# Kernel optimization log

Hardware: AMD Instinct MI355X
Metric: run time of the kernel (lower is better)

## Reference

```python
import jax, jax.numpy as jnp
import numpy as np

# dims
B, L, D = 2, 2048, 768
K, KQ, M = 12, 6, 4          # heads, query heads, thetas
H = D // K                    # 64 head dim (expand_factor=1)
NREP = K // KQ                # 2
MEM = K * H                   # 768
FLAT = K * H * M              # 3072
EXP = H * 3                   # 192 (out_expand_factor=3)
DSW = EXP * 2                 # 384 swiglu per head
LAT = D // 4                  # 192
CK = 4                        # conv kernel size
TH_MIN, TH_MAX = 1e-3, 3.0


def setup_inputs() -> dict:
    key = jax.random.key(0)
    ks = jax.random.split(key, 10)
    rn = lambda k, sh, s=0.02: jax.random.normal(k, sh, jnp.float32) * s
    # faithful parameter inits from the flax module
    grid_m = np.geomspace(TH_MIN, TH_MAX, M)
    theta_d_raw = jnp.asarray(
        np.log(np.exp(np.tile(grid_m.reshape(1, 1, 1, 1, M), (1, 1, K, H, 1))) - 1.0 + 1e-4),
        jnp.float32)
    decay_slopes = jnp.asarray(np.log(np.exp(np.geomspace(1e-3, 0.1, K)) - 1.0), jnp.float32)
    return {
        "x": jax.random.normal(ks[0], (B, L, D), jnp.float32),
        "W_mem": rn(ks[1], (D, MEM + K)),
        "conv_k": rn(ks[2], (CK, 1, MEM + K), 0.2),
        "W_q": rn(ks[3], (D, KQ * H * M * 2)),
        "theta_d_raw": theta_d_raw,
        "decay_slopes": decay_slopes,
        "score_scale": jnp.ones((K,), jnp.float32),
        "tanh_scale": jnp.ones((K,), jnp.float32),
        "W_re": rn(ks[4], (K, H, DSW), 0.05),
        "W_im": rn(ks[5], (K, H, DSW), 0.05),
        "norm_scale": jnp.ones((1, 1, K, H), jnp.float32),
        "gate_W": jnp.zeros((D, K), jnp.float32),
        "gate_b": jnp.full((K,), -3.0, jnp.float32),
        "skip_down_W": rn(ks[6], (D, LAT)),
        "skip_up_W": rn(ks[7], (LAT, K * DSW)),
        "highway_scale": jnp.ones((1, 1, K, 1), jnp.float32),
        "out_W": rn(ks[8], (K * EXP, D)),
    }


def reference(x, W_mem, conv_k, W_q, theta_d_raw, decay_slopes, score_scale, tanh_scale,
              W_re, W_im, norm_scale, gate_W, gate_b, skip_down_W, skip_up_W,
              highway_scale, out_W):
    b, l, _ = x.shape
    # memory stream: dense proj + depthwise causal conv
    z = x @ W_mem                                                     # (b,l,MEM+K)
    z = jax.lax.conv_general_dilated(z, conv_k, (1,), [(CK - 1, 0)],
                                     dimension_numbers=('NWC', 'WIO', 'NWC'),
                                     feature_group_count=MEM + K)
    k_val = z[..., :MEM].reshape(b, l, K, H)
    s_raw = z[..., MEM:].reshape(b, l, K, 1)
    q = (x @ W_q).reshape(b, l, KQ, H, M, 2)
    q_re, q_im = q[..., 0], q[..., 1]
    # multi-frequency theta grid + trapezoid quadrature weights
    theta_d = jax.nn.softplus(theta_d_raw) + 1e-4
    ta = jnp.cumsum(theta_d, axis=-1)
    total = ta[..., -1:]
    rng = TH_MAX - TH_MIN
    theta = TH_MIN + ta / total * rng                                 # (1,1,K,H,M)
    dth = (ta[..., 1:] - ta[..., :-1]) * (rng / total)
    w_int = jnp.concatenate([dth[..., :1] * 0.5,
                             0.5 * (dth[..., :-1] + dth[..., 1:]),
                             dth[..., -1:] * 0.5], axis=-1)           # (1,1,K,H,M)
    # ALiBi-like decay anchored at sequence end (all decay heads)
    pos = jnp.arange(l, dtype=jnp.float32)
    slopes = jax.nn.softplus(decay_slopes).reshape(1, 1, K, 1)
    dist = jnp.maximum(jnp.float32(l - 1) - pos, 0.0)
    log_tw = -slopes * dist[None, :, None, None]                      # (1,l,K,1)
    log_p = jnp.clip(score_scale[None, None, :, None] * s_raw, -20.0, 20.0)
    p_w = jnp.exp(log_p + log_tw)                                     # (b,l,K,1)
    # complex rotation of keys by per-head/per-freq phase
    kvw = k_val[..., None] * p_w[..., None]                           # (b,l,K,H,1)
    phi = jnp.tanh(tanh_scale.reshape(1, 1, K, 1, 1) * k_val[..., None]) * theta  # (b,l,K,H,M)
    re_k = kvw * jnp.cos(phi)
    im_k = kvw * jnp.sin(phi)
    # fused prefix-sum over time of (denominator, Re, Im)
    merged = jnp.concatenate([p_w[..., 0],
                              re_k.reshape(b, l, FLAT),
                              im_k.reshape(b, l, FLAT)], axis=-1)
    cs = jnp.cumsum(merged, axis=1)
    den, num_re, num_im = cs[..., :K], cs[..., K:K + FLAT], cs[..., K + FLAT:]
    inv_den = 1.0 / jnp.maximum(den[..., None], 1e-4)                 # (b,l,K,1)
    s_re = (num_re.reshape(b, l, K, H, M) * inv_den[..., None]).reshape(b, l, KQ, NREP, H, M)
    s_im = (num_im.reshape(b, l, K, H, M) * inv_den[..., None]).reshape(b, l, KQ, NREP, H, M)
    w_g = w_int.reshape(1, 1, KQ, NREP, H, M)
    qr, qi = q_re[:, :, :, None], q_im[:, :, :, None]                 # GQA broadcast over n_rep
    out_re = jnp.sum((s_re * qr + s_im * qi) * w_g, axis=-1).reshape(b, l, K, H)
    out_im = jnp.sum((s_im * qr - s_re * qi) * w_g, axis=-1).reshape(b, l, K, H)
    # gated spectral output + low-rank highway skip, swiglu, out proj
    gate = jax.nn.sigmoid(x @ gate_W + gate_b)[..., None]             # (b,l,K,1)
    y_re = jnp.einsum('blkh,khn->blkn', out_re * norm_scale, W_re)
    y_im = jnp.einsum('blkh,khn->blkn', out_im * norm_scale, W_im)
    y_spec = (y_re + y_im) * gate                                     # (b,l,K,DSW)
    y_dir = ((x @ skip_down_W) @ skip_up_W).reshape(b, l, K, DSW)
    yv_s, yg_s = jnp.split(y_spec, 2, axis=-1)
    yv_d, yg_d = jnp.split(y_dir, 2, axis=-1)
    y_val = yv_s + yv_d * highway_scale
    y_gate = yg_s + yg_d * highway_scale
    y = (y_val * jax.nn.silu(y_gate)).reshape(b, l, K * EXP)
    return y @ out_W
```

## Files before the change

kernel.cpp:

```cpp
#include <hip/hip_runtime.h>
#include <math.h>

#define B_    2
#define L_    2048
#define D_    768
#define K_    12
#define KQ_   6
#define M_    4
#define H_    64
#define ZC_   780
#define NTOK_ 4096
#define NC_   64
#define LC_   32
#define QST_  3072
#define XPN_  4096
#define ZOFF_ 3276

typedef __attribute__((ext_vector_type(8))) _Float16 half8;
typedef __attribute__((ext_vector_type(4))) float f32x4;

__device__ __forceinline__ float softplus_f(float x) {
  return (x > 20.f) ? x : log1pf(expf(x));
}

__device__ __forceinline__ float fast_tanh(float x) {
  float xx = fminf(fmaxf(x, -10.f), 10.f);
  float e = __expf(2.f * xx);
  return (e - 1.f) / (e + 1.f);
}

__device__ __forceinline__ void async16(const _Float16* g, _Float16* l) {
  __builtin_amdgcn_global_load_lds(
      (const __attribute__((address_space(1))) unsigned int*)g,
      (__attribute__((address_space(3))) unsigned int*)l, 16, 0, 0);
}

__device__ __forceinline__ int permcol(int n) {
  int isg = (n >= 192) ? 1 : 0;
  int j = n - 192 * isg;
  return (j >> 4) * 32 + (isg << 4) + (j & 15);
}

#define FENCE() asm volatile("" ::: "memory")

__device__ __forceinline__ void cvt_t_body(float (*tile)[33], int bx, int by, int kz,
                                           const float* src, long sKs, int srs,
                                           _Float16* dh, long dKs, int dst, int doff,
                                           int R, int Nact, int Nst, bool perm, float scale) {
  const float* s = src + (size_t)kz * sKs;
  _Float16* dhh = dh + (size_t)kz * dKs;
  const int kb = bx * 32;
  const int nb = by * 32;
  const int tx = threadIdx.x & 31, ty = threadIdx.x >> 5;
  for (int i = ty; i < 32; i += 8) {
    int kk = kb + i, n = nb + tx;
    tile[i][tx] = (kk < R && n < Nact) ? s[(size_t)kk * srs + n] : 0.f;
  }
  __syncthreads();
  for (int i = ty; i < 32; i += 8) {
    int n = nb + i, kk = kb + tx;
    if (kk < R && n < Nst) {
      float v = tile[tx][i] * scale;
      int dn = perm ? permcol(n) : n;
      dhh[(size_t)dn * dst + doff + kk] = (_Float16)v;
    }
  }
}

__global__ __launch_bounds__(256)
void prep_kernel(const float* __restrict__ x,
                 const float* __restrict__ W_mem, const float* __restrict__ W_q,
                 const float* __restrict__ skip_down_W, const float* __restrict__ out_W,
                 const float* __restrict__ W_re, const float* __restrict__ W_im,
                 const float* __restrict__ skip_up_W, const float* __restrict__ hs,
                 const float* __restrict__ gate_W,
                 const float* __restrict__ theta_d_raw, const float* __restrict__ decay,
                 _Float16* __restrict__ x_h,
                 _Float16* __restrict__ xpb_h, _Float16* __restrict__ outw_h,
                 _Float16* __restrict__ bsp_h,
                 float* __restrict__ theta_tab, float* __restrict__ w_tab,
                 float* __restrict__ slopes_sp) {
  __shared__ float tile[32][33];
  int b = blockIdx.x;
  if (b < 3) {
    int idx = b * 256 + threadIdx.x;
    if (idx < K_) slopes_sp[idx] = softplus_f(decay[idx]);
    if (idx >= K_ * H_) return;
    float td[M_], ta[M_];
#pragma unroll
    for (int m = 0; m < M_; ++m) td[m] = softplus_f(theta_d_raw[idx * M_ + m]) + 1e-4f;
    ta[0] = td[0];
#pragma unroll
    for (int m = 1; m < M_; ++m) ta[m] = ta[m - 1] + td[m];
    float total = ta[M_ - 1];
    float rs = 2.999f / total;
#pragma unroll
    for (int m = 0; m < M_; ++m) theta_tab[idx * M_ + m] = 0.001f + ta[m] * rs;
    float d0 = (ta[1] - ta[0]) * rs;
    float d1 = (ta[2] - ta[1]) * rs;
    float d2 = (ta[3] - ta[2]) * rs;
    w_tab[idx * M_ + 0] = 0.5f * d0;
    w_tab[idx * M_ + 1] = 0.5f * (d0 + d1);
    w_tab[idx * M_ + 2] = 0.5f * (d1 + d2);
    w_tab[idx * M_ + 3] = 0.5f * d2;
    return;
  }
  b -= 3;
  if (b < 6360) {
    if (b < 672) {
      cvt_t_body(tile, b % 24, b / 24, 0, W_mem, 0, ZC_, xpb_h + (size_t)ZOFF_ * 768,
                 0, 768, 0, 768, ZC_, ZC_, false, 1.f);
      return;
    }
    b -= 672;
    if (b < 2304) {
      cvt_t_body(tile, b % 24, b / 24, 0, W_q, 0, 3072, xpb_h, 0, 768, 0, 768,
                 3072, 3072, false, 1.f);
      return;
    }
    b -= 2304;
    if (b < 192) {
      cvt_t_body(tile, b % 24, b / 24, 0, skip_down_W, 0, 192, xpb_h + (size_t)3072 * 768,
                 0, 768, 0, 768, 192, 192, false, 1.f);
      return;
    }
    b -= 192;
    if (b < 1728) {
      cvt_t_body(tile, b % 72, b / 72, 0, out_W, 0, 768, outw_h, 0, 2304, 0, 2304,
                 768, 768, false, 1.f);
      return;
    }
    b -= 1728;
    if (b < 288) {
      cvt_t_body(tile, b % 2, (b / 2) % 12, b / 24, W_re, 64L * 384, 384, bsp_h,
                 384L * 320, 320, 0, 64, 384, 384, true, 1.f);
      return;
    }
    b -= 288;
    if (b < 288) {
      cvt_t_body(tile, b % 2, (b / 2) % 12, b / 24, W_im, 64L * 384, 384, bsp_h,
                 384L * 320, 320, 64, 64, 384, 384, true, 1.f);
      return;
    }
    b -= 288;
    if (b < 864) {
      int kz = b / 72;
      cvt_t_body(tile, b % 6, (b / 6) % 12, kz, skip_up_W, 384, 4608, bsp_h,
                 384L * 320, 320, 128, 192, 384, 384, true, hs[kz]);
      return;
    }
    b -= 864;
    cvt_t_body(tile, b, 0, 0, gate_W, 0, K_, xpb_h + (size_t)3264 * 768,
               0, 768, 0, 768, K_, K_, false, 1.f);
    return;
  }
  b -= 6360;
  size_t i = (size_t)b * 256 + threadIdx.x;
  if (i < (size_t)NTOK_ * D_) {
    x_h[i] = (_Float16)x[i];
  }
}

__global__ __launch_bounds__(512, 2)
void xproj256_kernel(const _Float16* __restrict__ Ah, const _Float16* __restrict__ Bh,
                     float* __restrict__ C, _Float16* __restrict__ YH,
                     _Float16* __restrict__ QH, float* __restrict__ GL) {
  __shared__ __align__(16) _Float16 sA[2][2][2][128][32];
  __shared__ __align__(16) _Float16 sB[2][2][2][128][32];

  const int bid = blockIdx.x;
  const int xcd = bid & 7, s = bid >> 3;
  const int by = xcd * 2 + (s & 1);
  const int bx = s >> 1;
  const int bm0 = by * 256, bn0 = bx * 256;

  const int tid = threadIdx.x;
  const int lane = tid & 63;
  const int wave = tid >> 6;
  const int m16 = lane & 15, quad = lane >> 4;
  const int wr = wave >> 2;
  const int wc = wave & 3;
  const int bhalf = wc >> 1;
  const int brow0 = (wc & 1) * 64;

  f32x4 acc[8][4];
#pragma unroll
  for (int i = 0; i < 8; ++i)
#pragma unroll
    for (int j = 0; j < 4; ++j) acc[i][j] = (f32x4){0.f, 0.f, 0.f, 0.f};

  const int sr = tid >> 2;
  const int lb = tid & 3;
  const int ssw = (sr >> 1) & 3;

  auto stageA = [&](int t, int h) {
    const int bb = t & 1;
    const _Float16* g = Ah + (size_t)(bm0 + h * 128 + sr) * 768 + t * 64
                        + ((lb ^ ssw) << 3);
    async16(g,      &sA[bb][h][0][0][0] + (size_t)tid * 8);
    async16(g + 32, &sA[bb][h][1][0][0] + (size_t)tid * 8);
  };
  auto stageB = [&](int t, int h) {
    const int bb = t & 1;
    const _Float16* g = Bh + (size_t)(bn0 + h * 128 + sr) * 768 + t * 64
                        + ((lb ^ ssw) << 3);
    async16(g,      &sB[bb][h][0][0][0] + (size_t)tid * 8);
    async16(g + 32, &sB[bb][h][1][0][0] + (size_t)tid * 8);
  };

  auto ldA = [&](int bb, int r, int kk) -> half8 {
    return *(const half8*)&sA[bb][wr][kk][r][(quad ^ ((r >> 1) & 3)) << 3];
  };
  auto ldB = [&](int bb, int r, int kk) -> half8 {
    return *(const half8*)&sB[bb][bhalf][kk][r][(quad ^ ((r >> 1) & 3)) << 3];
  };

  half8 aLo[8], aHi[8], bLo[4], bHi[4];

  stageB(0, 0); stageB(0, 1); stageA(0, 0); stageA(0, 1);
  stageB(1, 0); stageB(1, 1); stageA(1, 0); stageA(1, 1);
  __builtin_amdgcn_s_waitcnt(0x0F78);
  FENCE(); __builtin_amdgcn_s_barrier(); FENCE();
#pragma unroll
  for (int m = 0; m < 4; ++m)
#pragma unroll
    for (int kk = 0; kk < 2; ++kk) aLo[m * 2 + kk] = ldA(0, m * 16 + m16, kk);
#pragma unroll
  for (int n = 0; n < 2; ++n)
#pragma unroll
    for (int kk = 0; kk < 2; ++kk) bLo[n * 2 + kk] = ldB(0, brow0 + n * 16 + m16, kk);

  for (int t = 0; t < 12; ++t) {
    const int bb = t & 1;
    const int nb = bb ^ 1;
#pragma unroll
    for (int n = 0; n < 2; ++n)
#pragma unroll
      for (int kk = 0; kk < 2; ++kk)
        bHi[n * 2 + kk] = ldB(bb, brow0 + (n + 2) * 16 + m16, kk);
#pragma unroll
    for (int m = 0; m < 4; ++m)
#pragma unroll
      for (int kk = 0; kk < 2; ++kk)
        aHi[m * 2 + kk] = ldA(bb, 64 + m * 16 + m16, kk);
    FENCE(); __builtin_amdgcn_s_barrier(); FENCE();
    if (t < 10) { stageB(t + 2, 0); stageB(t + 2, 1); stageA(t + 2, 0); stageA(t + 2, 1); }
    FENCE();
    if (t < 10)
      __builtin_amdgcn_s_waitcnt(0x0F78);
    else
      __builtin_amdgcn_s_waitcnt(0x0F70);
    FENCE(); __builtin_amdgcn_s_barrier(); FENCE();
    __builtin_amdgcn_s_setprio(1);
#pragma unroll
    for (int kk = 0; kk < 2; ++kk)
#pragma unroll
      for (int m = 0; m < 4; ++m)
#pragma unroll
        for (int n = 0; n < 2; ++n)
          acc[m][n] = __builtin_amdgcn_mfma_f32_16x16x32_f16(aLo[m * 2 + kk], bLo[n * 2 + kk],
                                                             acc[m][n], 0, 0, 0);
#pragma unroll
    for (int kk = 0; kk < 2; ++kk)
#pragma unroll
      for (int m = 0; m < 4; ++m)
#pragma unroll
        for (int n = 2; n < 4; ++n)
          acc[m][n] = __builtin_amdgcn_mfma_f32_16x16x32_f16(aLo[m * 2 + kk], bHi[(n - 2) * 2 + kk],
                                                             acc[m][n], 0, 0, 0);
    __builtin_amdgcn_s_setprio(0);
    if (t < 11) {
#pragma unroll
      for (int m = 0; m < 4; ++m)
#pragma unroll
        for (int kk = 0; kk < 2; ++kk)
          aLo[m * 2 + kk] = ldA(nb, m * 16 + m16, kk);
    }
    __builtin_amdgcn_s_setprio(1);
#pragma unroll
    for (int kk = 0; kk < 2; ++kk)
#pragma unroll
      for (int m = 0; m < 4; ++m)
#pragma unroll
        for (int n = 0; n < 2; ++n)
          acc[m + 4][n] = __builtin_amdgcn_mfma_f32_16x16x32_f16(aHi[m * 2 + kk], bLo[n * 2 + kk],
                                                                 acc[m + 4][n], 0, 0, 0);
    __builtin_amdgcn_s_setprio(0);
    if (t < 11) {
#pragma unroll
      for (int n = 0; n < 2; ++n)
#pragma unroll
        for (int kk = 0; kk < 2; ++kk)
          bLo[n * 2 + kk] = ldB(nb, brow0 + n * 16 + m16, kk);
    }
    __builtin_amdgcn_s_setprio(1);
#pragma unroll
    for (int kk = 0; kk < 2; ++kk)
#pragma unroll
      for (int m = 0; m < 4; ++m)
#pragma unroll
        for (int n = 2; n < 4; ++n)
          acc[m + 4][n] = __builtin_amdgcn_mfma_f32_16x16x32_f16(aHi[m * 2 + kk], bHi[(n - 2) * 2 + kk],
                                                                 acc[m + 4][n], 0, 0, 0);
    __builtin_amdgcn_s_setprio(0);
  }

#pragma unroll
  for (int m = 0; m < 8; ++m) {
    const int row0 = bm0 + wr * 128 + m * 16 + quad * 4;
#pragma unroll
    for (int n = 0; n < 4; ++n) {
      const int col = bn0 + wc * 64 + n * 16 + m16;
      if (col < 3072) {
#pragma unroll
        for (int r = 0; r < 4; ++r)
          QH[(size_t)(row0 + r) * QST_ + col] = (_Float16)acc[m][n][r];
      } else if (col < 3264) {
        const int jj = col - 3072;
#pragma unroll
        for (int r = 0; r < 4; ++r)
          YH[(size_t)(row0 + r) * 192 + jj] = (_Float16)acc[m][n][r];
      } else if (col < 3276) {
        const int kk = col - 3264;
#pragma unroll
        for (int r = 0; r < 4; ++r)
          GL[(size_t)(row0 + r) * K_ + kk] = acc[m][n][r];
      } else if (col < 3276 + ZC_) {
        const int wz = col - ZOFF_;
#pragma unroll
        for (int r = 0; r < 4; ++r)
          C[(size_t)(row0 + r) * ZC_ + wz] = acc[m][n][r];
      }
    }
  }
}

__global__ __launch_bounds__(512, 2)
void outproj256_kernel(const _Float16* __restrict__ Ah, const _Float16* __restrict__ Bh,
                       float* __restrict__ out, float* __restrict__ part) {
  __shared__ __align__(16) _Float16 sA[2][2][2][128][32];
  __shared__ __align__(16) _Float16 sB[2][2][2][128][32];

  const int bid = blockIdx.x;
  const int xcd = bid & 7, s = bid >> 3;
  const int g = xcd * 24 + s;
  const int by = g & 15;
  const int c = g >> 4;
  const int kz_ = c / 3, bx = c - kz_ * 3;
  const int bm0 = by * 256, bn0 = bx * 256;
  const int kt0 = kz_ * 9;

  const int tid = threadIdx.x;
  const int lane = tid & 63;
  const int wave = tid >> 6;
  const int m16 = lane & 15, quad = lane >> 4;
  const int wr = wave >> 2;
  const int wc = wave & 3;
  const int bhalf = wc >> 1;
  const int brow0 = (wc & 1) * 64;

  f32x4 acc[8][4];
#pragma unroll
  for (int i = 0; i < 8; ++i)
#pragma unroll
    for (int j = 0; j < 4; ++j) acc[i][j] = (f32x4){0.f, 0.f, 0.f, 0.f};

  const int sr = tid >> 2;
  const int lbk = tid & 3;
  const int ssw = (sr >> 1) & 3;

  auto stageA = [&](int lt, int h) {
    const int bb = lt & 1;
    const _Float16* gp = Ah + (size_t)(bm0 + h * 128 + sr) * 2304 + (kt0 + lt) * 64
                         + ((lbk ^ ssw) << 3);
    async16(gp,      &sA[bb][h][0][0][0] + (size_t)tid * 8);
    async16(gp + 32, &sA[bb][h][1][0][0] + (size_t)tid * 8);
  };
  auto stageB = [&](int lt, int h) {
    const int bb = lt & 1;
    const _Float16* gp = Bh + (size_t)(bn0 + h * 128 + sr) * 2304 + (kt0 + lt) * 64
                         + ((lbk ^ ssw) << 3);
    async16(gp,      &sB[bb][h][0][0][0] + (size_t)tid * 8);
    async16(gp + 32, &sB[bb][h][1][0][0] + (size_t)tid * 8);
  };

  auto ldA = [&](int bb, int r, int kk) -> half8 {
    return *(const half8*)&sA[bb][wr][kk][r][(quad ^ ((r >> 1) & 3)) << 3];
  };
  auto ldB = [&](int bb, int r, int kk) -> half8 {
    return *(const half8*)&sB[bb][bhalf][kk][r][(quad ^ ((r >> 1) & 3)) << 3];
  };

  half8 aLo[8], aHi[8], bLo[4], bHi[4];

  stageB(0, 0); stageB(0, 1); stageA(0, 0); stageA(0, 1);
  stageB(1, 0); stageB(1, 1); stageA(1, 0); stageA(1, 1);
  __builtin_amdgcn_s_waitcnt(0x0F78);
  FENCE(); __builtin_amdgcn_s_barrier(); FENCE();
#pragma unroll
  for (int m = 0; m < 4; ++m)
#pragma unroll
    for (int kk = 0; kk < 2; ++kk) aLo[m * 2 + kk] = ldA(0, m * 16 + m16, kk);
#pragma unroll
  for (int n = 0; n < 2; ++n)
#pragma unroll
    for (int kk = 0; kk < 2; ++kk) bLo[n * 2 + kk] = ldB(0, brow0 + n * 16 + m16, kk);

  for (int t = 0; t < 9; ++t) {
    const int bb = t & 1;
    const int nb = bb ^ 1;
#pragma unroll
    for (int n = 0; n < 2; ++n)
#pragma unroll
      for (int kk = 0; kk < 2; ++kk)
        bHi[n * 2 + kk] = ldB(bb, brow0 + (n + 2) * 16 + m16, kk);
#pragma unroll
    for (int m = 0; m < 4; ++m)
#pragma unroll
      for (int kk = 0; kk < 2; ++kk)
        aHi[m * 2 + kk] = ldA(bb, 64 + m * 16 + m16, kk);
    FENCE(); __builtin_amdgcn_s_barrier(); FENCE();
    if (t < 7) { stageB(t + 2, 0); stageB(t + 2, 1); stageA(t + 2, 0); stageA(t + 2, 1); }
    FENCE();
    if (t < 7)
      __builtin_amdgcn_s_waitcnt(0x0F78);
    else
      __builtin_amdgcn_s_waitcnt(0x0F70);
    FENCE(); __builtin_amdgcn_s_barrier(); FENCE();
    __builtin_amdgcn_s_setprio(1);
#pragma unroll
    for (int kk = 0; kk < 2; ++kk)
#pragma unroll
      for (int m = 0; m < 4; ++m)
#pragma unroll
        for (int n = 0; n < 2; ++n)
          acc[m][n] = __builtin_amdgcn_mfma_f32_16x16x32_f16(aLo[m * 2 + kk], bLo[n * 2 + kk],
                                                             acc[m][n], 0, 0, 0);
#pragma unroll
    for (int kk = 0; kk < 2; ++kk)
#pragma unroll
      for (int m = 0; m < 4; ++m)
#pragma unroll
        for (int n = 2; n < 4; ++n)
          acc[m][n] = __builtin_amdgcn_mfma_f32_16x16x32_f16(aLo[m * 2 + kk], bHi[(n - 2) * 2 + kk],
                                                             acc[m][n], 0, 0, 0);
    __builtin_amdgcn_s_setprio(0);
    if (t < 8) {
#pragma unroll
      for (int m = 0; m < 4; ++m)
#pragma unroll
        for (int kk = 0; kk < 2; ++kk)
          aLo[m * 2 + kk] = ldA(nb, m * 16 + m16, kk);
    }
    __builtin_amdgcn_s_setprio(1);
#pragma unroll
    for (int kk = 0; kk < 2; ++kk)
#pragma unroll
      for (int m = 0; m < 4; ++m)
#pragma unroll
        for (int n = 0; n < 2; ++n)
          acc[m + 4][n] = __builtin_amdgcn_mfma_f32_16x16x32_f16(aHi[m * 2 + kk], bLo[n * 2 + kk],
                                                                 acc[m + 4][n], 0, 0, 0);
    __builtin_amdgcn_s_setprio(0);
    if (t < 8) {
#pragma unroll
      for (int n = 0; n < 2; ++n)
#pragma unroll
        for (int kk = 0; kk < 2; ++kk)
          bLo[n * 2 + kk] = ldB(nb, brow0 + n * 16 + m16, kk);
    }
    __builtin_amdgcn_s_setprio(1);
#pragma unroll
    for (int kk = 0; kk < 2; ++kk)
#pragma unroll
      for (int m = 0; m < 4; ++m)
#pragma unroll
        for (int n = 2; n < 4; ++n)
          acc[m + 4][n] = __builtin_amdgcn_mfma_f32_16x16x32_f16(aHi[m * 2 + kk], bHi[(n - 2) * 2 + kk],
                                                                 acc[m + 4][n], 0, 0, 0);
    __builtin_amdgcn_s_setprio(0);
  }

  float* dst = (kz_ == 0) ? out : part + (size_t)(kz_ - 1) * NTOK_ * 768;
#pragma unroll
  for (int m = 0; m < 8; ++m) {
    const int row0 = bm0 + wr * 128 + m * 16 + quad * 4;
#pragma unroll
    for (int n = 0; n < 4; ++n) {
      const int col = bn0 + wc * 64 + n * 16 + m16;
#pragma unroll
      for (int r = 0; r < 4; ++r)
        dst[(size_t)(row0 + r) * 768 + col] = acc[m][n][r];
    }
  }
}

__global__ __launch_bounds__(256)
void redout_kernel(float* __restrict__ o, const float* __restrict__ p) {
  const size_t i = (size_t)blockIdx.x * 256 + threadIdx.x;
  const f32x4* pv = (const f32x4*)p;
  f32x4 v = ((const f32x4*)o)[i];
  v += pv[i];
  v += pv[i + 786432];
  v += pv[i + 2 * 786432];
  ((f32x4*)o)[i] = v;
}

__global__ __launch_bounds__(256)
void spec_gemm_kernel(const _Float16* __restrict__ Ah, const _Float16* __restrict__ Bh,
                      const _Float16* __restrict__ A2, _Float16* __restrict__ YH) {
  __shared__ __align__(16) _Float16 sA[2][128 * 32];
  __shared__ __align__(16) _Float16 sB[2][128 * 32];
  const int Kd = 320;
  int bid = blockIdx.x;
  int xcd = bid & 7, s = bid >> 3;
  int kz = s / 12;
  int w = s % 12;
  int bx = w % 3;
  int by = (xcd << 2) + w / 3;
  const _Float16* A0 = Ah + (size_t)kz * ((size_t)NTOK_ * 128);
  const _Float16* B0 = Bh + (size_t)kz * (384L * 320);
  const int bm0 = by * 128;
  const int bn0 = bx * 128;
  const int tid = threadIdx.x;
  const int wave = tid >> 6, lane = tid & 63;
  const int m16 = lane & 15, quad = lane >> 4;
  const int wr = (wave & 1) * 64, wc = (wave >> 1) * 64;

  f32x4 acc[4][4];
#pragma unroll
  for (int i = 0; i < 4; ++i)
#pragma unroll
    for (int j = 0; j < 4; ++j) acc[i][j] = (f32x4){0.f, 0.f, 0.f, 0.f};

  const int lin = tid * 8;
  const int lrow = lin >> 5;
  const int lblk = (lin >> 3) & 3;
  const int csw = ((lblk ^ ((lrow >> 1) & 3)) << 3);

  auto stage = [&](int k0, int kb) {
    if (k0 < 128) {
      const _Float16* gA = A0 + (size_t)(bm0 + lrow) * 128 + (k0 + csw);
      async16(gA, &sA[kb][lin]);
      async16(gA + (size_t)64 * 128, &sA[kb][lin + 2048]);
    } else {
      const _Float16* gA = A2 + (size_t)(bm0 + lrow) * 192 + (k0 - 128 + csw);
      async16(gA, &sA[kb][lin]);
      async16(gA + (size_t)64 * 192, &sA[kb][lin + 2048]);
    }
    const _Float16* gB = B0 + (size_t)(bn0 + lrow) * Kd + (k0 + csw);
    async16(gB, &sB[kb][lin]);
    async16(gB + (size_t)64 * Kd, &sB[kb][lin + 2048]);
  };

  const int niter = Kd / 32;
  stage(0, 0);
  stage(32, 1);

  for (int it = 0; it < niter; ++it) {
    if (it == niter - 1)
      __builtin_amdgcn_s_waitcnt(0x0F70);
    else
      __builtin_amdgcn_s_waitcnt(0x0F74);
    __builtin_amdgcn_s_barrier();
    asm volatile("" ::: "memory");
    const int kb = it & 1;
    half8 a0[4], b0[4];
#pragma unroll
    for (int i = 0; i < 4; ++i) {
      const int rA = wr + i * 16 + m16;
      a0[i] = *(const half8*)&sA[kb][rA * 32 + ((quad ^ ((rA >> 1) & 3)) << 3)];
    }
#pragma unroll
    for (int j = 0; j < 4; ++j) {
      const int rB = wc + j * 16 + m16;
      b0[j] = *(const half8*)&sB[kb][rB * 32 + ((quad ^ ((rB >> 1) & 3)) << 3)];
    }
#pragma unroll
    for (int i = 0; i < 4; ++i)
#pragma unroll
      for (int j = 0; j < 4; ++j)
        acc[i][j] = __builtin_amdgcn_mfma_f32_16x16x32_f16(a0[i], b0[j], acc[i][j], 0, 0, 0);
    asm volatile("" ::: "memory");
    __builtin_amdgcn_s_barrier();
    asm volatile("" ::: "memory");
    if (it + 2 < niter) stage((it + 2) * 32, kb);
  }

#pragma unroll
  for (int i = 0; i < 4; ++i) {
    const int row0 = bm0 + wr + i * 16 + quad * 4;
#pragma unroll
    for (int j = 0; j < 4; j += 2) {
      const int colv = bn0 + wc + j * 16 + m16;
      const int jout = (colv >> 5) * 16 + m16;
#pragma unroll
      for (int r = 0; r < 4; ++r) {
        float val = acc[i][j][r];
        float gg = acc[i][j + 1][r];
        float sg = gg / (1.f + __expf(-gg));
        YH[(size_t)(row0 + r) * 2304 + kz * 192 + jout] = (_Float16)(val * sg);
      }
    }
  }
}

__global__ void pass_a_kernel(const float* __restrict__ zp,
                              const float* __restrict__ ck,
                              const float* __restrict__ theta_tab,
                              const float* __restrict__ score_scale,
                              const float* __restrict__ tanh_scale,
                              const float* __restrict__ slopes_sp,
                              float* __restrict__ csums) {
  const int c = blockIdx.x, k = blockIdx.y, b = blockIdx.z;
  const int tid = threadIdx.x;
  const int m = tid & 3, h = tid >> 2;
  const int chk = k * H_ + h;
  const int chs = 768 + k;
  const float theta_v = theta_tab[chk * M_ + m];
  const float ts = tanh_scale[k], ss = score_scale[k], slope = slopes_sp[k];
  float ckv[4], cks[4];
#pragma unroll
  for (int w = 0; w < 4; ++w) { ckv[w] = ck[w * ZC_ + chk]; cks[w] = ck[w * ZC_ + chs]; }
  const int l0 = c * LC_;
  float zk3 = 0.f, zk2 = 0.f, zk1 = 0.f, zs3 = 0.f, zs2 = 0.f, zs1 = 0.f;
#pragma unroll
  for (int p = 0; p < 3; ++p) {
    int lp = l0 - 3 + p;
    if (lp >= 0) {
      size_t tp = (size_t)b * L_ + lp;
      float zk = zp[tp * ZC_ + chk], zs = zp[tp * ZC_ + chs];
      if (p == 0) { zk3 = zk; zs3 = zs; }
      else if (p == 1) { zk2 = zk; zs2 = zs; }
      else { zk1 = zk; zs1 = zs; }
    }
  }
  float sre = 0.f, sim = 0.f, dacc = 0.f;
  for (int ll = 0; ll < LC_; ++ll) {
    int l = l0 + ll;
    size_t t = (size_t)b * L_ + l;
    float zk0 = zp[t * ZC_ + chk];
    float zs0 = zp[t * ZC_ + chs];
    float kv = zk3 * ckv[0] + zk2 * ckv[1] + zk1 * ckv[2] + zk0 * ckv[3];
    float sraw = zs3 * cks[0] + zs2 * cks[1] + zs1 * cks[2] + zs0 * cks[3];
    zk3 = zk2; zk2 = zk1; zk1 = zk0;
    zs3 = zs2; zs2 = zs1; zs1 = zs0;
    float lp = fminf(fmaxf(ss * sraw, -20.f), 20.f);
    float pw = __expf(lp - slope * (float)(L_ - 1 - l));
    float ph = fast_tanh(ts * kv) * theta_v;
    float kvp = kv * pw;
    sre += kvp * __cosf(ph);
    sim += kvp * __sinf(ph);
    dacc += pw;
  }
  size_t base = (((size_t)b * K_ + k) * NC_ + c) * 513;
  if (tid == 0) csums[base] = dacc;
  csums[base + 1 + h * 4 + m] = sre;
  csums[base + 1 + 256 + h * 4 + m] = sim;
}

__global__ void pass_b_kernel(const float* __restrict__ csums,
                              float* __restrict__ cpre) {
  int bk = blockIdx.y;
  int comp = blockIdx.x * 64 + threadIdx.x;
  if (comp >= 513) return;
  float run = 0.f;
  size_t base = (size_t)bk * NC_ * 513 + comp;
  for (int c = 0; c < NC_; ++c) {
    cpre[base + (size_t)c * 513] = run;
    run += csums[base + (size_t)c * 513];
  }
}

__global__ void pass_c_kernel(const float* __restrict__ zp,
                              const float* __restrict__ ck,
                              const _Float16* __restrict__ qh,
                              const float* __restrict__ theta_tab,
                              const float* __restrict__ w_tab,
                              const float* __restrict__ score_scale,
                              const float* __restrict__ tanh_scale,
                              const float* __restrict__ slopes_sp,
                              const float* __restrict__ cpre,
                              const float* __restrict__ gatelin,
                              const float* __restrict__ gate_b,
                              const float* __restrict__ ns,
                              _Float16* __restrict__ asp) {
  const int c = blockIdx.x, k = blockIdx.y, b = blockIdx.z;
  const int tid = threadIdx.x;
  const int m = tid & 3, h = tid >> 2;
  const int chk = k * H_ + h;
  const int chs = 768 + k;
  size_t base = (((size_t)b * K_ + k) * NC_ + c) * 513;
  float den = cpre[base];
  float sre = cpre[base + 1 + h * 4 + m];
  float sim = cpre[base + 1 + 256 + h * 4 + m];
  const float theta_v = theta_tab[chk * M_ + m];
  const float w = w_tab[chk * M_ + m];
  const float ts = tanh_scale[k], ss = score_scale[k], slope = slopes_sp[k];
  const float nsv = ns[chk];
  const float gb = gate_b[k];
  const int kq = k >> 1;
  float ckv[4], cks[4];
#pragma unroll
  for (int ww = 0; ww < 4; ++ww) { ckv[ww] = ck[ww * ZC_ + chk]; cks[ww] = ck[ww * ZC_ + chs]; }
  const int l0 = c * LC_;
  float zk3 = 0.f, zk2 = 0.f, zk1 = 0.f, zs3 = 0.f, zs2 = 0.f, zs1 = 0.f;
#pragma unroll
  for (int p = 0; p < 3; ++p) {
    int lp = l0 - 3 + p;
    if (lp >= 0) {
      size_t tp = (size_t)b * L_ + lp;
      float zk = zp[tp * ZC_ + chk], zs = zp[tp * ZC_ + chs];
      if (p == 0) { zk3 = zk; zs3 = zs; }
      else if (p == 1) { zk2 = zk; zs2 = zs; }
      else { zk1 = zk; zs1 = zs; }
    }
  }
  const int qidx = ((kq * H_ + h) * M_ + m) * 2;
  for (int ll = 0; ll < LC_; ++ll) {
    int l = l0 + ll;
    size_t t = (size_t)b * L_ + l;
    float zk0 = zp[t * ZC_ + chk];
    float zs0 = zp[t * ZC_ + chs];
    float kv = zk3 * ckv[0] + zk2 * ckv[1] + zk1 * ckv[2] + zk0 * ckv[3];
    float sraw = zs3 * cks[0] + zs2 * cks[1] + zs1 * cks[2] + zs0 * cks[3];
    zk3 = zk2; zk2 = zk1; zk1 = zk0;
    zs3 = zs2; zs2 = zs1; zs1 = zs0;
    float lp = fminf(fmaxf(ss * sraw, -20.f), 20.f);
    float pw = __expf(lp - slope * (float)(L_ - 1 - l));
    float ph = fast_tanh(ts * kv) * theta_v;
    float kvp = kv * pw;
    sre += kvp * __cosf(ph);
    sim += kvp * __sinf(ph);
    den += pw;
    float inv = 1.f / fmaxf(den, 1e-4f);
    float s_re = sre * inv, s_im = sim * inv;
    size_t qb = t * QST_ + qidx;
    float qr = (float)qh[qb], qi = (float)qh[qb + 1];
    float tr = (s_re * qr + s_im * qi) * w;
    float ti = (s_im * qr - s_re * qi) * w;
    tr += __shfl_xor(tr, 1); tr += __shfl_xor(tr, 2);
    ti += __shfl_xor(ti, 1); ti += __shfl_xor(ti, 2);
    if (m == 0) {
      float g = 1.f / (1.f + __expf(-(gatelin[t * K_ + k] + gb))) * nsv;
      size_t ab = ((size_t)k * NTOK_ + t) * 128;
      asp[ab + h] = (_Float16)(tr * g);
      asp[ab + 64 + h] = (_Float16)(ti * g);
    }
  }
}

extern "C" void kernel_launch(void* const* d_in, const int* in_sizes, int n_in,
                              void* d_out, int out_size, void* d_ws, size_t ws_size,
                              hipStream_t stream) {
  const float* x            = (const float*)d_in[0];
  const float* W_mem        = (const float*)d_in[1];
  const float* conv_k       = (const float*)d_in[2];
  const float* W_q          = (const float*)d_in[3];
  const float* theta_d_raw  = (const float*)d_in[4];
  const float* decay_slopes = (const float*)d_in[5];
  const float* score_scale  = (const float*)d_in[6];
  const float* tanh_scale   = (const float*)d_in[7];
  const float* W_re         = (const float*)d_in[8];
  const float* W_im         = (const float*)d_in[9];
  const float* norm_scale   = (const float*)d_in[10];
  const float* gate_W       = (const float*)d_in[11];
  const float* gate_b       = (const float*)d_in[12];
  const float* skip_down_W  = (const float*)d_in[13];
  const float* skip_up_W    = (const float*)d_in[14];
  const float* highway_scale= (const float*)d_in[15];
  const float* out_W        = (const float*)d_in[16];
  float* out = (float*)d_out;
  float* ws = (float*)d_ws;

  float* theta_tab = ws;
  float* w_tab     = theta_tab + 3072;
  float* slopes_sp = w_tab + 3072;
  float* z_pre     = slopes_sp + 16;
  float* gatelin   = z_pre + (size_t)NTOK_ * ZC_;
  float* csums     = gatelin + (size_t)NTOK_ * K_;
  float* cpre      = csums + (size_t)B_ * K_ * NC_ * 513;
  _Float16* q_h    = (_Float16*)(cpre + (size_t)B_ * K_ * NC_ * 513);
  _Float16* y_h    = q_h + (size_t)NTOK_ * QST_;
  float* f32_end   = (float*)(y_h + (size_t)NTOK_ * 2304);

  float* part = z_pre;

  _Float16* fp = (_Float16*)f32_end;
  _Float16* x_h    = fp;                fp += (size_t)NTOK_ * D_;
  _Float16* xpb_h  = fp;                fp += (size_t)XPN_ * 768;
  _Float16* outw_h = fp;                fp += (size_t)768 * 2304;
  _Float16* asp2_h = fp;                fp += (size_t)K_ * NTOK_ * 128;
  _Float16* bsp_h  = fp;                fp += (size_t)K_ * 384 * 320;
  _Float16* lat_h  = fp;                fp += (size_t)NTOK_ * 192;

  prep_kernel<<<18651, 256, 0, stream>>>(x, W_mem, W_q, skip_down_W, out_W, W_re, W_im,
                                         skip_up_W, highway_scale, gate_W,
                                         theta_d_raw, decay_slopes,
                                         x_h, xpb_h, outw_h, bsp_h,
                                         theta_tab, w_tab, slopes_sp);

  xproj256_kernel<<<256, 512, 0, stream>>>(x_h, xpb_h, z_pre, lat_h, q_h, gatelin);

  pass_a_kernel<<<dim3(NC_, K_, B_), 256, 0, stream>>>(z_pre, conv_k, theta_tab, score_scale,
                                                       tanh_scale, slopes_sp, csums);
  pass_b_kernel<<<dim3(9, B_ * K_), 64, 0, stream>>>(csums, cpre);
  pass_c_kernel<<<dim3(NC_, K_, B_), 256, 0, stream>>>(z_pre, conv_k, q_h, theta_tab, w_tab,
                                                       score_scale, tanh_scale, slopes_sp, cpre,
                                                       gatelin, gate_b, norm_scale, asp2_h);

  spec_gemm_kernel<<<1152, 256, 0, stream>>>(asp2_h, bsp_h, lat_h, y_h);

  outproj256_kernel<<<192, 512, 0, stream>>>(y_h, outw_h, out, part);
  redout_kernel<<<3072, 256, 0, stream>>>(out, part);
}
```

Baseline: 278.8 us.

## Precompute conv, decay weights and tanh phases in shared memory for scan passes

Pass A and pass C now compute the per-token score weights, running denominator (via warp prefix scan), gate sigmoid, conv outputs and tanh phases once per block into shared memory. Previously every thread redundantly recomputed them: the four m lanes each recomputed kv and tanh, and all threads recomputed the score conv and exp. The per-thread scan loop then reads these from LDS. This adds a __syncthreads and LDS traffic, and serializes a small prologue on the first warp.

```diff
diff --git a/kernel.cpp b/kernel.cpp
--- a/kernel.cpp
+++ b/kernel.cpp
@@ -605,56 +605,88 @@
   }
 }
 
-__global__ void pass_a_kernel(const float* __restrict__ zp,
-                              const float* __restrict__ ck,
-                              const float* __restrict__ theta_tab,
-                              const float* __restrict__ score_scale,
-                              const float* __restrict__ tanh_scale,
-                              const float* __restrict__ slopes_sp,
-                              float* __restrict__ csums) {
+__global__ __launch_bounds__(256)
+void pass_a_kernel(const float* __restrict__ zp,
+                   const float* __restrict__ ck,
+                   const float* __restrict__ theta_tab,
+                   const float* __restrict__ score_scale,
+                   const float* __restrict__ tanh_scale,
+                   const float* __restrict__ slopes_sp,
+                   float* __restrict__ csums) {
   const int c = blockIdx.x, k = blockIdx.y, b = blockIdx.z;
   const int tid = threadIdx.x;
   const int m = tid & 3, h = tid >> 2;
+  const int l0 = c * LC_;
+  const size_t base = (((size_t)b * K_ + k) * NC_ + c) * 513;
+
+  __shared__ float s_pw[LC_];
+  __shared__ float s_kv[LC_][H_];
+  __shared__ float s_th[LC_][H_];
+
+  if (tid < 32) {
+    const int chs = 768 + k;
+    const float ss = score_scale[k], slope = slopes_sp[k];
+    float cks[4];
+#pragma unroll
+    for (int w = 0; w < 4; ++w) cks[w] = ck[w * ZC_ + chs];
+    float sraw = 0.f;
+#pragma unroll
+    for (int j = 0; j < 4; ++j) {
+      int lp_ = l0 + tid - 3 + j;
+      float zs = (lp_ >= 0) ? zp[((size_t)b * L_ + lp_) * ZC_ + chs] : 0.f;
+      sraw += zs * cks[j];
+    }
+    float lp = fminf(fmaxf(ss * sraw, -20.f), 20.f);
+    int l = l0 + tid;
+    float pw = __expf(lp - slope * (float)(L_ - 1 - l));
+    s_pw[tid] = pw;
+    float tot = pw;
+    tot += __shfl_xor(tot, 1);
+    tot += __shfl_xor(tot, 2);
+    tot += __shfl_xor(tot, 4);
+    tot += __shfl_xor(tot, 8);
+    tot += __shfl_xor(tot, 16);
+    if (tid == 0) csums[base] = tot;
+  }
+
+  {
+    const int hh = tid >> 2, g = tid & 3;
+    const int chkh = k * H_ + hh;
+    const float ts = tanh_scale[k];
+    float ckv[4];
+#pragma unroll
+    for (int w = 0; w < 4; ++w) ckv[w] = ck[w * ZC_ + chkh];
+    const int lbase = l0 + g * 8;
+    float z3 = 0.f, z2 = 0.f, z1 = 0.f;
+#pragma unroll
+    for (int p = 0; p < 3; ++p) {
+      int lp_ = lbase - 3 + p;
+      if (lp_ >= 0) {
+        float z = zp[((size_t)b * L_ + lp_) * ZC_ + chkh];
+        if (p == 0) z3 = z; else if (p == 1) z2 = z; else z1 = z;
+      }
+    }
+#pragma unroll
+    for (int j = 0; j < 8; ++j) {
+      float z0 = zp[((size_t)b * L_ + lbase + j) * ZC_ + chkh];
+      float kv = z3 * ckv[0] + z2 * ckv[1] + z1 * ckv[2] + z0 * ckv[3];
+      z3 = z2; z2 = z1; z1 = z0;
+      s_kv[g * 8 + j][hh] = kv;
+      s_th[g * 8 + j][hh] = fast_tanh(ts * kv);
+    }
+  }
+  __syncthreads();
+
   const int chk = k * H_ + h;
-  const int chs = 768 + k;
   const float theta_v = theta_tab[chk * M_ + m];
-  const float ts = tanh_scale[k], ss = score_scale[k], slope = slopes_sp[k];
-  float ckv[4], cks[4];
-#pragma unroll
-  for (int w = 0; w < 4; ++w) { ckv[w] = ck[w * ZC_ + chk]; cks[w] = ck[w * ZC_ + chs]; }
-  const int l0 = c * LC_;
-  float zk3 = 0.f, zk2 = 0.f, zk1 = 0.f, zs3 = 0.f, zs2 = 0.f, zs1 = 0.f;
-#pragma unroll
-  for (int p = 0; p < 3; ++p) {
-    int lp = l0 - 3 + p;
-    if (lp >= 0) {
-      size_t tp = (size_t)b * L_ + lp;
-      float zk = zp[tp * ZC_ + chk], zs = zp[tp * ZC_ + chs];
-      if (p == 0) { zk3 = zk; zs3 = zs; }
-      else if (p == 1) { zk2 = zk; zs2 = zs; }
-      else { zk1 = zk; zs1 = zs; }
-    }
-  }
-  float sre = 0.f, sim = 0.f, dacc = 0.f;
+  float sre = 0.f, sim = 0.f;
+#pragma unroll 8
   for (int ll = 0; ll < LC_; ++ll) {
-    int l = l0 + ll;
-    size_t t = (size_t)b * L_ + l;
-    float zk0 = zp[t * ZC_ + chk];
-    float zs0 = zp[t * ZC_ + chs];
-    float kv = zk3 * ckv[0] + zk2 * ckv[1] + zk1 * ckv[2] + zk0 * ckv[3];
-    float sraw = zs3 * cks[0] + zs2 * cks[1] + zs1 * cks[2] + zs0 * cks[3];
-    zk3 = zk2; zk2 = zk1; zk1 = zk0;
-    zs3 = zs2; zs2 = zs1; zs1 = zs0;
-    float lp = fminf(fmaxf(ss * sraw, -20.f), 20.f);
-    float pw = __expf(lp - slope * (float)(L_ - 1 - l));
-    float ph = fast_tanh(ts * kv) * theta_v;
-    float kvp = kv * pw;
+    float kvp = s_kv[ll][h] * s_pw[ll];
+    float ph = s_th[ll][h] * theta_v;
     sre += kvp * __cosf(ph);
     sim += kvp * __sinf(ph);
-    dacc += pw;
-  }
-  size_t base = (((size_t)b * K_ + k) * NC_ + c) * 513;
-  if (tid == 0) csums[base] = dacc;
+  }
   csums[base + 1 + h * 4 + m] = sre;
   csums[base + 1 + 256 + h * 4 + m] = sim;
 }
@@ -666,75 +698,114 @@
   if (comp >= 513) return;
   float run = 0.f;
   size_t base = (size_t)bk * NC_ * 513 + comp;
+#pragma unroll 4
   for (int c = 0; c < NC_; ++c) {
     cpre[base + (size_t)c * 513] = run;
     run += csums[base + (size_t)c * 513];
   }
 }
 
-__global__ void pass_c_kernel(const float* __restrict__ zp,
-                              const float* __restrict__ ck,
-                              const _Float16* __restrict__ qh,
-                              const float* __restrict__ theta_tab,
-                              const float* __restrict__ w_tab,
-                              const float* __restrict__ score_scale,
-                              const float* __restrict__ tanh_scale,
-                              const float* __restrict__ slopes_sp,
-                              const float* __restrict__ cpre,
-                              const float* __restrict__ gatelin,
-                              const float* __restrict__ gate_b,
-                              const float* __restrict__ ns,
-                              _Float16* __restrict__ asp) {
+__global__ __launch_bounds__(256)
+void pass_c_kernel(const float* __restrict__ zp,
+                   const float* __restrict__ ck,
+                   const _Float16* __restrict__ qh,
+                   const float* __restrict__ theta_tab,
+                   const float* __restrict__ w_tab,
+                   const float* __restrict__ score_scale,
+                   const float* __restrict__ tanh_scale,
+                   const float* __restrict__ slopes_sp,
+                   const float* __restrict__ cpre,
+                   const float* __restrict__ gatelin,
+                   const float* __restrict__ gate_b,
+                   const float* __restrict__ ns,
+                   _Float16* __restrict__ asp) {
   const int c = blockIdx.x, k = blockIdx.y, b = blockIdx.z;
   const int tid = threadIdx.x;
   const int m = tid & 3, h = tid >> 2;
+  const int l0 = c * LC_;
+  const size_t base = (((size_t)b * K_ + k) * NC_ + c) * 513;
+
+  __shared__ float s_pw[LC_];
+  __shared__ float s_inv[LC_];
+  __shared__ float s_sg[LC_];
+  __shared__ float s_kv[LC_][H_];
+  __shared__ float s_th[LC_][H_];
+
+  if (tid < 32) {
+    const int chs = 768 + k;
+    const float ss = score_scale[k], slope = slopes_sp[k];
+    const float gb = gate_b[k];
+    float cks[4];
+#pragma unroll
+    for (int w = 0; w < 4; ++w) cks[w] = ck[w * ZC_ + chs];
+    float sraw = 0.f;
+#pragma unroll
+    for (int j = 0; j < 4; ++j) {
+      int lp_ = l0 + tid - 3 + j;
+      float zs = (lp_ >= 0) ? zp[((size_t)b * L_ + lp_) * ZC_ + chs] : 0.f;
+      sraw += zs * cks[j];
+    }
+    float lp = fminf(fmaxf(ss * sraw, -20.f), 20.f);
+    int l = l0 + tid;
+    float pw = __expf(lp - slope * (float)(L_ - 1 - l));
+    s_pw[tid] = pw;
+    float pref = pw;
+#pragma unroll
+    for (int off = 1; off < 32; off <<= 1) {
+      float nv = __shfl_up(pref, off);
+      if (tid >= off) pref += nv;
+    }
+    float den = cpre[base] + pref;
+    s_inv[tid] = 1.f / fmaxf(den, 1e-4f);
+    float gl = gatelin[((size_t)b * L_ + l) * K_ + k];
+    s_sg[tid] = 1.f / (1.f + __expf(-(gl + gb)));
+  }
+
+  {
+    const int hh = tid >> 2, g = tid & 3;
+    const int chkh = k * H_ + hh;
+    const float ts = tanh_scale[k];
+    float ckv[4];
+#pragma unroll
+    for (int w = 0; w < 4; ++w) ckv[w] = ck[w * ZC_ + chkh];
+    const int lbase = l0 + g * 8;
+    float z3 = 0.f, z2 = 0.f, z1 = 0.f;
+#pragma unroll
+    for (int p = 0; p < 3; ++p) {
+      int lp_ = lbase - 3 + p;
+      if (lp_ >= 0) {
+        float z = zp[((size_t)b * L_ + lp_) * ZC_ + chkh];
+        if (p == 0) z3 = z; else if (p == 1) z2 = z; else z1 = z;
+      }
+    }
+#pragma unroll
+    for (int j = 0; j < 8; ++j) {
+      float z0 = zp[((size_t)b * L_ + lbase + j) * ZC_ + chkh];
+      float kv = z3 * ckv[0] + z2 * ckv[1] + z1 * ckv[2] + z0 * ckv[3];
+      z3 = z2; z2 = z1; z1 = z0;
+      s_kv[g * 8 + j][hh] = kv;
+      s_th[g * 8 + j][hh] = fast_tanh(ts * kv);
+    }
+  }
+  __syncthreads();
+
   const int chk = k * H_ + h;
-  const int chs = 768 + k;
-  size_t base = (((size_t)b * K_ + k) * NC_ + c) * 513;
-  float den = cpre[base];
+  const float theta_v = theta_tab[chk * M_ + m];
+  const float w = w_tab[chk * M_ + m];
+  const float nsv = ns[chk];
+  const int kq = k >> 1;
+  const int qidx = ((kq * H_ + h) * M_ + m) * 2;
   float sre = cpre[base + 1 + h * 4 + m];
   float sim = cpre[base + 1 + 256 + h * 4 + m];
-  const float theta_v = theta_tab[chk * M_ + m];
-  const float w = w_tab[chk * M_ + m];
-  const float ts = tanh_scale[k], ss = score_scale[k], slope = slopes_sp[k];
-  const float nsv = ns[chk];
-  const float gb = gate_b[k];
-  const int kq = k >> 1;
-  float ckv[4], cks[4];
-#pragma unroll
-  for (int ww = 0; ww < 4; ++ww) { ckv[ww] = ck[ww * ZC_ + chk]; cks[ww] = ck[ww * ZC_ + chs]; }
-  const int l0 = c * LC_;
-  float zk3 = 0.f, zk2 = 0.f, zk1 = 0.f, zs3 = 0.f, zs2 = 0.f, zs1 = 0.f;
-#pragma unroll
-  for (int p = 0; p < 3; ++p) {
-    int lp = l0 - 3 + p;
-    if (lp >= 0) {
-      size_t tp = (size_t)b * L_ + lp;
-      float zk = zp[tp * ZC_ + chk], zs = zp[tp * ZC_ + chs];
-      if (p == 0) { zk3 = zk; zs3 = zs; }
-      else if (p == 1) { zk2 = zk; zs2 = zs; }
-      else { zk1 = zk; zs1 = zs; }
-    }
-  }
-  const int qidx = ((kq * H_ + h) * M_ + m) * 2;
+#pragma unroll 4
   for (int ll = 0; ll < LC_; ++ll) {
-    int l = l0 + ll;
-    size_t t = (size_t)b * L_ + l;
-    float zk0 = zp[t * ZC_ + chk];
-    float zs0 = zp[t * ZC_ + chs];
-    float kv = zk3 * ckv[0] + zk2 * ckv[1] + zk1 * ckv[2] + zk0 * ckv[3];
-    float sraw = zs3 * cks[0] + zs2 * cks[1] + zs1 * cks[2] + zs0 * cks[3];
-    zk3 = zk2; zk2 = zk1; zk1 = zk0;
-    zs3 = zs2; zs2 = zs1; zs1 = zs0;
-    float lp = fminf(fmaxf(ss * sraw, -20.f), 20.f);
-    float pw = __expf(lp - slope * (float)(L_ - 1 - l));
-    float ph = fast_tanh(ts * kv) * theta_v;
-    float kvp = kv * pw;
+    float kvp = s_kv[ll][h] * s_pw[ll];
+    float ph = s_th[ll][h] * theta_v;
     sre += kvp * __cosf(ph);
     sim += kvp * __sinf(ph);
-    den += pw;
-    float inv = 1.f / fmaxf(den, 1e-4f);
+    float inv = s_inv[ll];
     float s_re = sre * inv, s_im = sim * inv;
+    size_t t = (size_t)b * L_ + l0 + ll;
     size_t qb = t * QST_ + qidx;
     float qr = (float)qh[qb], qi = (float)qh[qb + 1];
     float tr = (s_re * qr + s_im * qi) * w;
@@ -742,7 +813,7 @@
     tr += __shfl_xor(tr, 1); tr += __shfl_xor(tr, 2);
     ti += __shfl_xor(ti, 1); ti += __shfl_xor(ti, 2);
     if (m == 0) {
-      float g = 1.f / (1.f + __expf(-(gatelin[t * K_ + k] + gb))) * nsv;
+      float g = s_sg[ll] * nsv;
       size_t ab = ((size_t)k * NTOK_ + t) * 128;
       asp[ab + h] = (_Float16)(tr * g);
       asp[ab + 64 + h] = (_Float16)(ti * g);
```

Measured after the change: 253.0 us. 9.3% less time.
